# Performance work log

Hardware: AMD Instinct MI355X
Metric: run time of the kernel (lower is better)

The kernel has to match this reference:

```python
import jax, jax.numpy as jnp
import numpy as np

DEC_H = 1024
ENC_H_TOTAL = 1024  # enc_hid_size * enc_num_dirs


def setup_inputs() -> dict:
    key = jax.random.key(0)
    ks = jax.random.split(key, 10)
    N, L = 64, 1024
    s = 0.02
    return {
        "dec_h_curr": jax.random.normal(ks[0], (N, DEC_H), jnp.float32),
        "enc_hids": jax.random.normal(ks[1], (N, L, ENC_H_TOTAL), jnp.float32),
        # project_dec_hids: Linear(dec_H, dec_H)
        "W_dec": jax.random.normal(ks[2], (DEC_H, DEC_H), jnp.float32) * s,
        "b_dec": jnp.zeros((DEC_H,), jnp.float32),
        # project_enc_hids: Linear(enc_H*nDir, dec_H)
        "W_enc": jax.random.normal(ks[3], (ENC_H_TOTAL, DEC_H), jnp.float32) * s,
        "b_enc": jnp.zeros((DEC_H,), jnp.float32),
        # project_to_one_dim: Linear(dec_H, 1)
        "W_one": jax.random.normal(ks[4], (DEC_H, 1), jnp.float32) * s,
        "b_one": jnp.zeros((1,), jnp.float32),
        # project_att_hids: Linear(enc_H*nDir, dec_H)
        "W_att": jax.random.normal(ks[5], (ENC_H_TOTAL, DEC_H), jnp.float32) * s,
        "b_att": jnp.zeros((DEC_H,), jnp.float32),
    }


def reference(dec_h_curr, enc_hids, W_dec, b_dec, W_enc, b_enc, W_one, b_one, W_att, b_att):
    # additive (Bahdanau) attention branch
    d = dec_h_curr @ W_dec + b_dec                     # N x dec_H
    e = jnp.einsum('nle,ed->nld', enc_hids, W_enc) + b_enc  # N x L x dec_H
    scores = jnp.einsum('nld,do->nl', jnp.tanh(d[:, None, :] + e), W_one) + b_one[0]  # N x L
    alpha = jax.nn.softmax(scores, axis=-1)            # N x L
    ctx = jnp.einsum('nl,nle->ne', alpha, enc_hids)    # N x enc_H_total
    h_att_curr = ctx @ W_att + b_att                   # N x dec_H
    return h_att_curr, alpha
```

## Files before the change

### kernel.cpp

```cpp
#include <hip/hip_runtime.h>
#include <cstdio>
#include <cstdint>


typedef __bf16 bf16x8 __attribute__((ext_vector_type(8)));
typedef float f32x4 __attribute__((ext_vector_type(4)));
typedef unsigned short us8 __attribute__((ext_vector_type(8)));

static __device__ __forceinline__ unsigned short f2b(float f) {
  union { float f; unsigned u; } v; v.f = f;
  unsigned r = (v.u + 0x7fffu + ((v.u >> 16) & 1u)) >> 16;
  return (unsigned short)r;
}
static __device__ __forceinline__ float b2f(unsigned short u) {
  union { unsigned u; float f; } v; v.u = ((unsigned)u) << 16;
  return v.f;
}
static __device__ __forceinline__ void gl_lds16(const void* g, void* l) {
  __builtin_amdgcn_global_load_lds(
      (const __attribute__((address_space(1))) unsigned int*)g,
      (__attribute__((address_space(3))) unsigned int*)l, 16, 0, 0);
}
static __device__ __forceinline__ float fast_tanh(float x) {
  float ax = __builtin_fminf(__builtin_fabsf(x), 18.0f);
  float u = __builtin_amdgcn_exp2f(ax * 2.88539008177792681f);
  float t = (u - 1.0f) * __builtin_amdgcn_rcpf(u + 1.0f);
  return __builtin_copysignf(t, x);
}

__global__ __launch_bounds__(256) void pack_a(const float* __restrict__ enc,
                                              unsigned short* __restrict__ Ap) {
  __shared__ __align__(16) unsigned short tile[128 * 72];
  const int bid = blockIdx.x;
  const int T = bid >> 4, kt = bid & 15;
  const int t = threadIdx.x;
  #pragma unroll
  for (int it = 0; it < 8; ++it) {
    int idx = it * 256 + t;
    int m = idx >> 4, c4 = idx & 15;
    const float4 v = *(const float4*)(enc + (size_t)(T * 128 + m) * 1024 + kt * 64 + c4 * 4);
    ushort4 o;
    o.x = f2b(v.x); o.y = f2b(v.y); o.z = f2b(v.z); o.w = f2b(v.w);
    *(ushort4*)&tile[m * 72 + c4 * 4] = o;
  }
  __syncthreads();
  #pragma unroll
  for (int it = 0; it < 4; ++it) {
    int p = it * 256 + t;
    int c = p >> 7, m = p & 127;
    us8 v = *(const us8*)&tile[m * 72 + c * 8];
    *(us8*)(Ap + ((size_t)bid * 1024 + p) * 8) = v;
  }
}

__global__ __launch_bounds__(256) void pack_b(const float* __restrict__ W,
                                              unsigned short* __restrict__ Bp) {
  __shared__ __align__(16) unsigned short tile[128 * 72];
  const int bid = blockIdx.x;
  const int Tn = bid >> 4, kt = bid & 15;
  const int t = threadIdx.x;
  #pragma unroll
  for (int it = 0; it < 8; ++it) {
    int idx = it * 256 + t;
    int kk = idx >> 5, n4 = idx & 31;
    const float4 v = *(const float4*)(W + (size_t)(kt * 64 + kk) * 1024 + Tn * 128 + n4 * 4);
    tile[(n4 * 4 + 0) * 72 + kk] = f2b(v.x);
    tile[(n4 * 4 + 1) * 72 + kk] = f2b(v.y);
    tile[(n4 * 4 + 2) * 72 + kk] = f2b(v.z);
    tile[(n4 * 4 + 3) * 72 + kk] = f2b(v.w);
  }
  __syncthreads();
  #pragma unroll
  for (int it = 0; it < 4; ++it) {
    int p = it * 256 + t;
    int c = p >> 7, m = p & 127;
    us8 v = *(const us8*)&tile[m * 72 + c * 8];
    *(us8*)(Bp + ((size_t)bid * 1024 + p) * 8) = v;
  }
}

__global__ void dterm_k(const float* __restrict__ dec_h, const float* __restrict__ W_dec,
                        const float* __restrict__ b_dec, const float* __restrict__ b_enc,
                        float* __restrict__ addterm) {
  __shared__ float xs[1024];
  int n = blockIdx.y;
  int j = blockIdx.x * 256 + threadIdx.x;
  for (int i = threadIdx.x; i < 1024; i += 256) xs[i] = dec_h[n * 1024 + i];
  __syncthreads();
  float s = 0.f;
  #pragma unroll 8
  for (int k = 0; k < 1024; ++k) s += xs[k] * W_dec[(size_t)k * 1024 + j];
  addterm[n * 1024 + j] = s + b_dec[j] + b_enc[j];
}

__global__ __launch_bounds__(256) void score_gemm(
    const unsigned short* __restrict__ Ap, const unsigned short* __restrict__ Bp,
    const float* __restrict__ addterm, const float* __restrict__ Wone,
    float* __restrict__ spart) {
  __shared__ __align__(16) unsigned short lA[8192];
  __shared__ __align__(16) unsigned short lB[8192];
  const int tid = threadIdx.x;
  const int lane = tid & 63, wave = tid >> 6;
  const int wm = wave >> 1, wn = wave & 1;
  const int q = lane >> 4, r = lane & 15;
  const int flat = blockIdx.x;
  const int nb = (flat >> 3) & 7;
  const int mb = ((flat >> 6) << 3) + (flat & 7);
  const size_t tileM = (size_t)mb * 128;
  const int tileN = nb * 128;

  f32x4 acc[4][4];
  #pragma unroll
  for (int i = 0; i < 4; ++i)
    #pragma unroll
    for (int j = 0; j < 4; ++j) acc[i][j] = (f32x4){0.f, 0.f, 0.f, 0.f};

  const unsigned short* gA[2][2];
  const unsigned short* gB[2][2];
  unsigned short* dA[2][2];
  unsigned short* dB[2][2];
  #pragma unroll
  for (int cc = 0; cc < 2; ++cc) {
    int c = wave * 2 + cc;
    #pragma unroll
    for (int i = 0; i < 2; ++i) {
      gA[cc][i] = Ap + ((((size_t)mb * 16) * 8 + c) * 128 + i * 64 + lane) * 8;
      gB[cc][i] = Bp + ((((size_t)nb * 16) * 8 + c) * 128 + i * 64 + lane) * 8;
      dA[cc][i] = &lA[(c * 128 + i * 64) * 8];
      dB[cc][i] = &lB[(c * 128 + i * 64) * 8];
    }
  }

  for (int kt = 0; kt < 16; ++kt) {
    __syncthreads();
    const size_t ko = (size_t)kt * 8192;
    gl_lds16(gA[0][0] + ko, dA[0][0]);
    gl_lds16(gA[0][1] + ko, dA[0][1]);
    gl_lds16(gA[1][0] + ko, dA[1][0]);
    gl_lds16(gA[1][1] + ko, dA[1][1]);
    gl_lds16(gB[0][0] + ko, dB[0][0]);
    gl_lds16(gB[0][1] + ko, dB[0][1]);
    gl_lds16(gB[1][0] + ko, dB[1][0]);
    gl_lds16(gB[1][1] + ko, dB[1][1]);
    __syncthreads();
    #pragma unroll
    for (int s = 0; s < 2; ++s) {
      bf16x8 af[4], bg[4];
      #pragma unroll
      for (int mi = 0; mi < 4; ++mi)
        af[mi] = *(const bf16x8*)&lA[((s * 4 + q) * 128 + wm * 64 + mi * 16 + r) * 8];
      #pragma unroll
      for (int ni = 0; ni < 4; ++ni)
        bg[ni] = *(const bf16x8*)&lB[((s * 4 + q) * 128 + wn * 64 + ni * 16 + r) * 8];
      #pragma unroll
      for (int mi = 0; mi < 4; ++mi)
        #pragma unroll
        for (int ni = 0; ni < 4; ++ni)
          acc[mi][ni] = __builtin_amdgcn_mfma_f32_16x16x32_bf16(af[mi], bg[ni], acc[mi][ni], 0, 0, 0);
    }
  }

  const int nrow = (int)(tileM >> 10);
  float addv[4], wv[4];
  #pragma unroll
  for (int ni = 0; ni < 4; ++ni) {
    int col = tileN + wn * 64 + ni * 16 + r;
    addv[ni] = addterm[nrow * 1024 + col];
    wv[ni] = Wone[col];
  }
  #pragma unroll
  for (int mi = 0; mi < 4; ++mi) {
    #pragma unroll
    for (int rr = 0; rr < 4; ++rr) {
      float s = 0.f;
      #pragma unroll
      for (int ni = 0; ni < 4; ++ni)
        s += fast_tanh(acc[mi][ni][rr] + addv[ni]) * wv[ni];
      s += __shfl_xor(s, 1);
      s += __shfl_xor(s, 2);
      s += __shfl_xor(s, 4);
      s += __shfl_xor(s, 8);
      if (r == 0) {
        size_t row = tileM + wm * 64 + mi * 16 + q * 4 + rr;
        spart[row * 16 + nb * 2 + wn] = s;
      }
    }
  }
}

__global__ void softmax_k(const float* __restrict__ spart, float* __restrict__ alpha) {
  int n = blockIdx.x, t = threadIdx.x;
  __shared__ float red[8];
  float sv[4];
  #pragma unroll
  for (int i = 0; i < 4; ++i) {
    int l = i * 256 + t;
    const float4* p = (const float4*)(spart + ((size_t)n * 1024 + l) * 16);
    float4 v0 = p[0], v1 = p[1], v2 = p[2], v3 = p[3];
    sv[i] = (v0.x + v0.y + v0.z + v0.w) + (v1.x + v1.y + v1.z + v1.w) +
            (v2.x + v2.y + v2.z + v2.w) + (v3.x + v3.y + v3.z + v3.w);
  }
  float m = fmaxf(fmaxf(sv[0], sv[1]), fmaxf(sv[2], sv[3]));
  for (int o = 32; o > 0; o >>= 1) m = fmaxf(m, __shfl_xor(m, o));
  if ((t & 63) == 0) red[t >> 6] = m;
  __syncthreads();
  float gm = fmaxf(fmaxf(red[0], red[1]), fmaxf(red[2], red[3]));
  float e[4], s = 0.f;
  #pragma unroll
  for (int i = 0; i < 4; ++i) { e[i] = expf(sv[i] - gm); s += e[i]; }
  for (int o = 32; o > 0; o >>= 1) s += __shfl_xor(s, o);
  if ((t & 63) == 0) red[4 + (t >> 6)] = s;
  __syncthreads();
  float inv = 1.0f / (red[4] + red[5] + red[6] + red[7]);
  #pragma unroll
  for (int i = 0; i < 4; ++i) alpha[(size_t)n * 1024 + i * 256 + t] = e[i] * inv;
}

__global__ void ctx_k(const unsigned short* __restrict__ Ap, const float* __restrict__ alpha,
                      float* __restrict__ ctx) {
  const int kt = blockIdx.x, n = blockIdx.y, t = threadIdx.x;
  __shared__ float al[1024];
  for (int i = t; i < 1024; i += 256) al[i] = alpha[n * 1024 + i];
  __syncthreads();
  const int c = t >> 5, ls = t & 31;
  float acc[8] = {0.f, 0.f, 0.f, 0.f, 0.f, 0.f, 0.f, 0.f};
  #pragma unroll 4
  for (int lb = 0; lb < 32; ++lb) {
    int l = lb * 32 + ls;
    int M = n * 1024 + l;
    int T = M >> 7, m = M & 127;
    us8 v = *(const us8*)(Ap + ((((size_t)T * 16 + kt) * 8 + c) * 128 + m) * 8);
    float w = al[l];
    #pragma unroll
    for (int j = 0; j < 8; ++j) acc[j] += w * b2f(v[j]);
  }
  #pragma unroll
  for (int off = 1; off <= 16; off <<= 1)
    #pragma unroll
    for (int j = 0; j < 8; ++j) acc[j] += __shfl_xor(acc[j], off);
  if (ls == 0) {
    #pragma unroll
    for (int j = 0; j < 8; ++j) ctx[(size_t)n * 1024 + kt * 64 + c * 8 + j] = acc[j];
  }
}

__global__ void hatt_k(const float* __restrict__ ctx, const float* __restrict__ W_att,
                       const float* __restrict__ b_att, float* __restrict__ out) {
  __shared__ float cs[1024];
  int n = blockIdx.y;
  int j = blockIdx.x * 256 + threadIdx.x;
  for (int i = threadIdx.x; i < 1024; i += 256) cs[i] = ctx[(size_t)n * 1024 + i];
  __syncthreads();
  float s = 0.f;
  #pragma unroll 8
  for (int k = 0; k < 1024; ++k) s += cs[k] * W_att[(size_t)k * 1024 + j];
  out[n * 1024 + j] = s + b_att[j];
}

extern "C" void kernel_launch(void* const* d_in, const int* in_sizes, int n_in,
                              void* d_out, int out_size, void* d_ws, size_t ws_size,
                              hipStream_t stream) {
  const float* dec_h = (const float*)d_in[0];
  const float* enc   = (const float*)d_in[1];
  const float* W_dec = (const float*)d_in[2];
  const float* b_dec = (const float*)d_in[3];
  const float* W_enc = (const float*)d_in[4];
  const float* b_enc = (const float*)d_in[5];
  const float* W_one = (const float*)d_in[6];
  const float* W_att = (const float*)d_in[8];
  const float* b_att = (const float*)d_in[9];
  float* out = (float*)d_out;

  char* ws = (char*)d_ws;
  const size_t OFF_A   = 0;
  const size_t OFF_B   = 134217728;
  const size_t OFF_ADD = OFF_B + 2097152;
  const size_t OFF_SP  = OFF_ADD + 262144;
  const size_t OFF_CTX = OFF_SP + 4194304;
  const size_t NEED    = OFF_CTX + 262144;
  if (ws_size < NEED) {
    fprintf(stderr, "kernel_launch: ws too small (%zu < %zu)\n", ws_size, NEED);
    return;
  }
  unsigned short* Ap = (unsigned short*)(ws + OFF_A);
  unsigned short* Bp = (unsigned short*)(ws + OFF_B);
  float* addterm = (float*)(ws + OFF_ADD);
  float* spart   = (float*)(ws + OFF_SP);
  float* ctx     = (float*)(ws + OFF_CTX);
  float* alpha   = out + 65536;

  pack_a<<<8192, 256, 0, stream>>>(enc, Ap);
  pack_b<<<128, 256, 0, stream>>>(W_enc, Bp);
  dterm_k<<<dim3(4, 64), 256, 0, stream>>>(dec_h, W_dec, b_dec, b_enc, addterm);
  score_gemm<<<4096, 256, 0, stream>>>(Ap, Bp, addterm, W_one, spart);
  softmax_k<<<64, 256, 0, stream>>>(spart, alpha);
  ctx_k<<<dim3(16, 64), 256, 0, stream>>>(Ap, alpha, ctx);
  hatt_k<<<dim3(4, 64), 256, 0, stream>>>(ctx, W_att, b_att, out);
}
```

Measured before the change: 713.9 us.

## Merge pack and dterm kernels into one launch, fuse softmax into ctx

Combines pack_a, pack_b and dterm_k into a single prep kernel that dispatches on block index, so three launches become one and the small jobs share the GPU with the large pack. The LDS staging tile switches from a padded layout to an XOR-swizzled one to avoid bank conflicts. Softmax is fused into the ctx kernel: each of the 16 blocks per row recomputes the softmax from spart, and only kt==0 writes alpha. This removes launches and the alpha round trip through memory, at the cost of reading spart 16 times.

```diff
diff --git a/kernel.cpp b/kernel.cpp
--- a/kernel.cpp
+++ b/kernel.cpp
@@ -28,69 +28,72 @@
   return __builtin_copysignf(t, x);
 }
 
-__global__ __launch_bounds__(256) void pack_a(const float* __restrict__ enc,
-                                              unsigned short* __restrict__ Ap) {
-  __shared__ __align__(16) unsigned short tile[128 * 72];
+__global__ __launch_bounds__(256) void prep_k(
+    const float* __restrict__ enc, unsigned short* __restrict__ Ap,
+    const float* __restrict__ W_enc, unsigned short* __restrict__ Bp,
+    const float* __restrict__ dec_h, const float* __restrict__ W_dec,
+    const float* __restrict__ b_dec, const float* __restrict__ b_enc,
+    float* __restrict__ addterm) {
+  __shared__ __align__(16) unsigned short tile[8192];
   const int bid = blockIdx.x;
-  const int T = bid >> 4, kt = bid & 15;
   const int t = threadIdx.x;
-  #pragma unroll
-  for (int it = 0; it < 8; ++it) {
-    int idx = it * 256 + t;
-    int m = idx >> 4, c4 = idx & 15;
-    const float4 v = *(const float4*)(enc + (size_t)(T * 128 + m) * 1024 + kt * 64 + c4 * 4);
-    ushort4 o;
-    o.x = f2b(v.x); o.y = f2b(v.y); o.z = f2b(v.z); o.w = f2b(v.w);
-    *(ushort4*)&tile[m * 72 + c4 * 4] = o;
-  }
-  __syncthreads();
-  #pragma unroll
-  for (int it = 0; it < 4; ++it) {
-    int p = it * 256 + t;
-    int c = p >> 7, m = p & 127;
-    us8 v = *(const us8*)&tile[m * 72 + c * 8];
-    *(us8*)(Ap + ((size_t)bid * 1024 + p) * 8) = v;
-  }
-}
-
-__global__ __launch_bounds__(256) void pack_b(const float* __restrict__ W,
-                                              unsigned short* __restrict__ Bp) {
-  __shared__ __align__(16) unsigned short tile[128 * 72];
-  const int bid = blockIdx.x;
-  const int Tn = bid >> 4, kt = bid & 15;
-  const int t = threadIdx.x;
-  #pragma unroll
-  for (int it = 0; it < 8; ++it) {
-    int idx = it * 256 + t;
-    int kk = idx >> 5, n4 = idx & 31;
-    const float4 v = *(const float4*)(W + (size_t)(kt * 64 + kk) * 1024 + Tn * 128 + n4 * 4);
-    tile[(n4 * 4 + 0) * 72 + kk] = f2b(v.x);
-    tile[(n4 * 4 + 1) * 72 + kk] = f2b(v.y);
-    tile[(n4 * 4 + 2) * 72 + kk] = f2b(v.z);
-    tile[(n4 * 4 + 3) * 72 + kk] = f2b(v.w);
-  }
-  __syncthreads();
-  #pragma unroll
-  for (int it = 0; it < 4; ++it) {
-    int p = it * 256 + t;
-    int c = p >> 7, m = p & 127;
-    us8 v = *(const us8*)&tile[m * 72 + c * 8];
-    *(us8*)(Bp + ((size_t)bid * 1024 + p) * 8) = v;
-  }
-}
-
-__global__ void dterm_k(const float* __restrict__ dec_h, const float* __restrict__ W_dec,
-                        const float* __restrict__ b_dec, const float* __restrict__ b_enc,
-                        float* __restrict__ addterm) {
-  __shared__ float xs[1024];
-  int n = blockIdx.y;
-  int j = blockIdx.x * 256 + threadIdx.x;
-  for (int i = threadIdx.x; i < 1024; i += 256) xs[i] = dec_h[n * 1024 + i];
-  __syncthreads();
-  float s = 0.f;
-  #pragma unroll 8
-  for (int k = 0; k < 1024; ++k) s += xs[k] * W_dec[(size_t)k * 1024 + j];
-  addterm[n * 1024 + j] = s + b_dec[j] + b_enc[j];
+
+  if (bid < 128) {
+    const int Tn = bid >> 4, kt = bid & 15;
+    #pragma unroll
+    for (int it = 0; it < 8; ++it) {
+      int idx = it * 256 + t;
+      int kk = idx >> 5, n4 = idx & 31;
+      const float4 v = *(const float4*)(W_enc + (size_t)(kt * 64 + kk) * 1024 + Tn * 128 + n4 * 4);
+      int c = kk >> 3, j = kk & 7;
+      #pragma unroll
+      for (int x = 0; x < 4; ++x) {
+        int mm = n4 * 4 + x;
+        float fv = (x == 0) ? v.x : (x == 1) ? v.y : (x == 2) ? v.z : v.w;
+        tile[(mm * 8 + (c ^ (mm & 7))) * 8 + j] = f2b(fv);
+      }
+    }
+    __syncthreads();
+    #pragma unroll
+    for (int it = 0; it < 4; ++it) {
+      int p = it * 256 + t;
+      int c = p >> 7, m = p & 127;
+      us8 v = *(const us8*)&tile[(m * 8 + (c ^ (m & 7))) * 8];
+      *(us8*)(Bp + ((size_t)bid * 1024 + p) * 8) = v;
+    }
+  } else if (bid < 384) {
+    const int bid2 = bid - 128;
+    const int jb = bid2 & 3, n = bid2 >> 2;
+    float* xs = (float*)tile;
+    for (int i = t; i < 1024; i += 256) xs[i] = dec_h[n * 1024 + i];
+    __syncthreads();
+    int j = jb * 256 + t;
+    float s = 0.f;
+    #pragma unroll 8
+    for (int k = 0; k < 1024; ++k) s += xs[k] * W_dec[(size_t)k * 1024 + j];
+    addterm[n * 1024 + j] = s + b_dec[j] + b_enc[j];
+  } else {
+    const int ba = bid - 384;
+    const int T = ba >> 4, kt = ba & 15;
+    #pragma unroll
+    for (int it = 0; it < 8; ++it) {
+      int idx = it * 256 + t;
+      int m = idx >> 4, c4 = idx & 15;
+      const float4 v = *(const float4*)(enc + (size_t)(T * 128 + m) * 1024 + kt * 64 + c4 * 4);
+      ushort4 o;
+      o.x = f2b(v.x); o.y = f2b(v.y); o.z = f2b(v.z); o.w = f2b(v.w);
+      int c = c4 >> 1, half = c4 & 1;
+      *(ushort4*)&tile[(m * 8 + (c ^ (m & 7))) * 8 + half * 4] = o;
+    }
+    __syncthreads();
+    #pragma unroll
+    for (int it = 0; it < 4; ++it) {
+      int p = it * 256 + t;
+      int c = p >> 7, m = p & 127;
+      us8 v = *(const us8*)&tile[(m * 8 + (c ^ (m & 7))) * 8];
+      *(us8*)(Ap + ((size_t)ba * 1024 + p) * 8) = v;
+    }
+  }
 }
 
 __global__ __launch_bounds__(256) void score_gemm(
@@ -188,9 +191,13 @@
   }
 }
 
-__global__ void softmax_k(const float* __restrict__ spart, float* __restrict__ alpha) {
-  int n = blockIdx.x, t = threadIdx.x;
+__global__ __launch_bounds__(256) void ctx_fused(
+    const float* __restrict__ spart, float* __restrict__ alpha,
+    const unsigned short* __restrict__ Ap, float* __restrict__ ctx) {
+  const int kt = blockIdx.x, n = blockIdx.y, t = threadIdx.x;
   __shared__ float red[8];
+  __shared__ float al[1024];
+
   float sv[4];
   #pragma unroll
   for (int i = 0; i < 4; ++i) {
@@ -213,23 +220,21 @@
   __syncthreads();
   float inv = 1.0f / (red[4] + red[5] + red[6] + red[7]);
   #pragma unroll
-  for (int i = 0; i < 4; ++i) alpha[(size_t)n * 1024 + i * 256 + t] = e[i] * inv;
-}
-
-__global__ void ctx_k(const unsigned short* __restrict__ Ap, const float* __restrict__ alpha,
-                      float* __restrict__ ctx) {
-  const int kt = blockIdx.x, n = blockIdx.y, t = threadIdx.x;
-  __shared__ float al[1024];
-  for (int i = t; i < 1024; i += 256) al[i] = alpha[n * 1024 + i];
+  for (int i = 0; i < 4; ++i) {
+    float a = e[i] * inv;
+    al[i * 256 + t] = a;
+    if (kt == 0) alpha[(size_t)n * 1024 + i * 256 + t] = a;
+  }
   __syncthreads();
+
   const int c = t >> 5, ls = t & 31;
   float acc[8] = {0.f, 0.f, 0.f, 0.f, 0.f, 0.f, 0.f, 0.f};
   #pragma unroll 4
   for (int lb = 0; lb < 32; ++lb) {
     int l = lb * 32 + ls;
     int M = n * 1024 + l;
-    int T = M >> 7, m = M & 127;
-    us8 v = *(const us8*)(Ap + ((((size_t)T * 16 + kt) * 8 + c) * 128 + m) * 8);
+    int T = M >> 7, mm = M & 127;
+    us8 v = *(const us8*)(Ap + ((((size_t)T * 16 + kt) * 8 + c) * 128 + mm) * 8);
     float w = al[l];
     #pragma unroll
     for (int j = 0; j < 8; ++j) acc[j] += w * b2f(v[j]);
@@ -289,11 +294,8 @@
   float* ctx     = (float*)(ws + OFF_CTX);
   float* alpha   = out + 65536;
 
-  pack_a<<<8192, 256, 0, stream>>>(enc, Ap);
-  pack_b<<<128, 256, 0, stream>>>(W_enc, Bp);
-  dterm_k<<<dim3(4, 64), 256, 0, stream>>>(dec_h, W_dec, b_dec, b_enc, addterm);
+  prep_k<<<8576, 256, 0, stream>>>(enc, Ap, W_enc, Bp, dec_h, W_dec, b_dec, b_enc, addterm);
   score_gemm<<<4096, 256, 0, stream>>>(Ap, Bp, addterm, W_one, spart);
-  softmax_k<<<64, 256, 0, stream>>>(spart, alpha);
-  ctx_k<<<dim3(16, 64), 256, 0, stream>>>(Ap, alpha, ctx);
+  ctx_fused<<<dim3(16, 64), 256, 0, stream>>>(spart, alpha, Ap, ctx);
   hatt_k<<<dim3(4, 64), 256, 0, stream>>>(ctx, W_att, b_att, out);
 }
```

Result: faster. 689.0 us (-3.5%).
